# Kernel optimization log

Hardware: AMD Instinct MI355X
Metric: run time of the kernel (lower is better)

Reference implementation:

```python
import jax, jax.numpy as jnp
import numpy as np

B, T, C, H = 4, 2048, 1024, 16
D = C // H          # head_dim = 64
FF = 2 * C          # ff_mult = 2
EPS = 1e-5


def _layernorm(x, g, b):
    mu = jnp.mean(x, axis=-1, keepdims=True)
    var = jnp.mean((x - mu) ** 2, axis=-1, keepdims=True)
    return (x - mu) * jax.lax.rsqrt(var + EPS) * g + b


def setup_inputs() -> dict:
    key = jax.random.key(0)
    ks = jax.random.split(key, 8)
    x = jax.random.normal(ks[0], (B, T, C), dtype=jnp.float32)
    perm = jax.random.permutation(ks[1], T).astype(jnp.int32)
    s_c = 1.0 / np.sqrt(C)
    s_f = 1.0 / np.sqrt(FF)
    Wqkv = jax.random.normal(ks[2], (C, 3 * C), dtype=jnp.float32) * s_c
    Wproj = jax.random.normal(ks[3], (C, C), dtype=jnp.float32) * s_c
    bproj = jnp.zeros((C,), dtype=jnp.float32)
    ln1_g = jnp.ones((C,), dtype=jnp.float32)
    ln1_b = jnp.zeros((C,), dtype=jnp.float32)
    ln2_g = jnp.ones((C,), dtype=jnp.float32)
    ln2_b = jnp.zeros((C,), dtype=jnp.float32)
    Wff1 = jax.random.normal(ks[4], (C, FF), dtype=jnp.float32) * s_c
    bff1 = jnp.zeros((FF,), dtype=jnp.float32)
    Wff2 = jax.random.normal(ks[5], (FF, C), dtype=jnp.float32) * s_f
    bff2 = jnp.zeros((C,), dtype=jnp.float32)
    return {"x": x, "perm": perm, "Wqkv": Wqkv, "Wproj": Wproj, "bproj": bproj,
            "ln1_g": ln1_g, "ln1_b": ln1_b, "ln2_g": ln2_g, "ln2_b": ln2_b,
            "Wff1": Wff1, "bff1": bff1, "Wff2": Wff2, "bff2": bff2}


def reference(x, perm, Wqkv, Wproj, bproj, ln1_g, ln1_b, ln2_g, ln2_b,
              Wff1, bff1, Wff2, bff2):
    # --- attention branch ---
    h = _layernorm(x, ln1_g, ln1_b)                       # [B,T,C]
    qkv = (h @ Wqkv).reshape(B, T, 3, H, D)
    q, k, v = qkv[:, :, 0], qkv[:, :, 1], qkv[:, :, 2]    # [B,T,H,D]
    # random-permuted causal additive mask: masked = ~tril[:, perm]
    rows = jnp.arange(T)[:, None]
    masked = perm[None, :] > rows                          # [T,T] bool
    bias = jnp.where(masked, -jnp.inf, 0.0).astype(x.dtype)
    scale = 1.0 / np.sqrt(D)
    scores = jnp.einsum('bqhd,bkhd->bhqk', q, k) * scale + bias
    attn = jax.nn.softmax(scores, axis=-1)                 # [B,H,T,T]
    y = jnp.einsum('bhqk,bkhd->bqhd', attn, v).reshape(B, T, C)
    x = x + y @ Wproj + bproj
    # --- MLP branch ---
    h2 = _layernorm(x, ln2_g, ln2_b)
    ff = jax.nn.gelu(h2 @ Wff1 + bff1, approximate=False) @ Wff2 + bff2
    return x + ff
```

## Files before the change

kernel.cpp:

```cpp
#include <hip/hip_runtime.h>
#include <math.h>

#define Bb 4
#define Tt 2048
#define Cc 1024
#define Hh 16
#define Dd 64
#define FFf 2048
#define Mrows (Bb*Tt)

typedef _Float16 f16;
typedef _Float16 half8 __attribute__((ext_vector_type(8)));
typedef _Float16 half4 __attribute__((ext_vector_type(4)));
typedef _Float16 half2 __attribute__((ext_vector_type(2)));
typedef __fp16 fp16x2 __attribute__((ext_vector_type(2)));
typedef float floatx4 __attribute__((ext_vector_type(4)));

#define MFMA16(a,b,c)    __builtin_amdgcn_mfma_f32_16x16x32_f16(a,b,c,0,0,0)
#define MFMA16K16(a,b,c) __builtin_amdgcn_mfma_f32_16x16x16f16(a,b,c,0,0,0)

__device__ __forceinline__ void g2l16(const void* g, void* l) {
  __builtin_amdgcn_global_load_lds((__attribute__((address_space(1))) void*)(g),
                                   (__attribute__((address_space(3))) void*)(l),
                                   16, 0, 0);
}

__global__ __launch_bounds__(256) void wt_kernel(const float* __restrict__ W,
                                                 f16* __restrict__ WT,
                                                 const int K, const int N) {
  __shared__ float tile[32][33];
  const int n0 = blockIdx.x * 32, k0 = blockIdx.y * 32;
  const int tx = threadIdx.x, ty = threadIdx.y;
  #pragma unroll
  for (int i = 0; i < 4; i++)
    tile[ty + 8*i][tx] = W[(size_t)(k0 + ty + 8*i) * N + n0 + tx];
  __syncthreads();
  #pragma unroll
  for (int i = 0; i < 4; i++)
    WT[(size_t)(n0 + ty + 8*i) * K + k0 + tx] = (f16)tile[tx][ty + 8*i];
}

__global__ __launch_bounds__(256) void vt_kernel(const f16* __restrict__ V,
                                                 f16* __restrict__ Vt) {
  __shared__ f16 tile[32][33];
  const int bh = blockIdx.z;
  const int t0 = blockIdx.x * 32, d0 = blockIdx.y * 32;
  const int tx = threadIdx.x, ty = threadIdx.y;
  #pragma unroll
  for (int i = 0; i < 4; i++)
    tile[ty + 8*i][tx] = V[((size_t)bh * Tt + t0 + ty + 8*i) * Dd + d0 + tx];
  __syncthreads();
  #pragma unroll
  for (int i = 0; i < 4; i++)
    Vt[((size_t)bh * Dd + d0 + ty + 8*i) * Tt + t0 + tx] = tile[tx][ty + 8*i];
}

__global__ __launch_bounds__(256) void ln_kernel(const float* __restrict__ x,
                                                 const float* __restrict__ gam,
                                                 const float* __restrict__ bet,
                                                 f16* __restrict__ out) {
  const int row = blockIdx.x;
  const int tid = threadIdx.x;
  const float4 v = ((const float4*)(x + (size_t)row * Cc))[tid];
  float s  = v.x + v.y + v.z + v.w;
  float ss = v.x*v.x + v.y*v.y + v.z*v.z + v.w*v.w;
  #pragma unroll
  for (int o = 32; o >= 1; o >>= 1) { s += __shfl_xor(s, o); ss += __shfl_xor(ss, o); }
  __shared__ float ps[4], pss[4];
  if ((tid & 63) == 0) { ps[tid >> 6] = s; pss[tid >> 6] = ss; }
  __syncthreads();
  s  = ps[0] + ps[1] + ps[2] + ps[3];
  ss = pss[0] + pss[1] + pss[2] + pss[3];
  const float mu   = s * (1.0f / Cc);
  const float rstd = rsqrtf(ss * (1.0f / Cc) - mu * mu + 1e-5f);
  const float4 g4 = ((const float4*)gam)[tid];
  const float4 b4 = ((const float4*)bet)[tid];
  half4 o;
  o[0] = (f16)((v.x - mu) * rstd * g4.x + b4.x);
  o[1] = (f16)((v.y - mu) * rstd * g4.y + b4.y);
  o[2] = (f16)((v.z - mu) * rstd * g4.z + b4.z);
  o[3] = (f16)((v.w - mu) * rstd * g4.w + b4.w);
  ((half4*)(out + (size_t)row * Cc))[tid] = o;
}

template <int MODE>
__global__ __launch_bounds__(256, 2) void gemm_kernel(
    const f16* __restrict__ A, const f16* __restrict__ Bt, const int Kdim,
    const float* __restrict__ resid, const float* __restrict__ bias,
    float* __restrict__ outF, f16* __restrict__ outH,
    f16* __restrict__ outQ, f16* __restrict__ outK, f16* __restrict__ outV) {
  __shared__ f16 As[128 * 32];
  __shared__ f16 Bs[128 * 32];
  const int tid = threadIdx.x;
  const int lane = tid & 63;
  const int w = tid >> 6;
  const int wr = w >> 1, wc = w & 1;
  const int bm = blockIdx.y, bn = blockIdx.x;

  floatx4 acc[4][4] = {};

  const size_t aBase = (size_t)(bm*128 + w*32 + (lane >> 2)) * Kdim + (lane & 3) * 8;
  const size_t bBase = (size_t)(bn*128 + w*32 + (lane >> 2)) * Kdim + (lane & 3) * 8;

  for (int ks = 0; ks < Kdim; ks += 32) {
    __syncthreads();
    g2l16(A  + aBase + ks,                    &As[(w*2 + 0) * 512]);
    g2l16(A  + aBase + (size_t)16*Kdim + ks,  &As[(w*2 + 1) * 512]);
    g2l16(Bt + bBase + ks,                    &Bs[(w*2 + 0) * 512]);
    g2l16(Bt + bBase + (size_t)16*Kdim + ks,  &Bs[(w*2 + 1) * 512]);
    __syncthreads();
    half8 aF[4], bF[4];
    #pragma unroll
    for (int mi = 0; mi < 4; mi++)
      aF[mi] = *(const half8*)&As[(wr*64 + mi*16 + (lane & 15)) * 32 + (lane >> 4) * 8];
    #pragma unroll
    for (int ni = 0; ni < 4; ni++)
      bF[ni] = *(const half8*)&Bs[(wc*64 + ni*16 + (lane & 15)) * 32 + (lane >> 4) * 8];
    #pragma unroll
    for (int mi = 0; mi < 4; mi++)
      #pragma unroll
      for (int ni = 0; ni < 4; ni++)
        acc[mi][ni] = MFMA16(aF[mi], bF[ni], acc[mi][ni]);
  }

  const int rowBase = bm*128 + wr*64;
  const int colBase = bn*128 + wc*64;
  #pragma unroll
  for (int mi = 0; mi < 4; mi++) {
    #pragma unroll
    for (int ni = 0; ni < 4; ni++) {
      #pragma unroll
      for (int r = 0; r < 4; r++) {
        const int row = rowBase + mi*16 + (lane >> 4) * 4 + r;
        const int col = colBase + ni*16 + (lane & 15);
        const float vv = acc[mi][ni][r];
        if (MODE == 0) {
          const int s = col >> 10;
          const int hh = (col >> 6) & 15;
          const int d = col & 63;
          const int bI = row >> 11;
          const int t = row & 2047;
          const size_t addr = (((size_t)(bI*Hh + hh)) * Tt + t) * Dd + d;
          f16* dst = (s == 0) ? outQ : (s == 1 ? outK : outV);
          dst[addr] = (f16)(s == 0 ? vv * 0.18033688f : vv);
        } else if (MODE == 1) {
          const size_t a = (size_t)row * Cc + col;
          outF[a] = vv + resid[a] + bias[col];
        } else if (MODE == 2) {
          const float t = vv + bias[col];
          const float gl = 0.5f * t * (1.0f + erff(t * 0.70710678118654752f));
          outH[(size_t)row * FFf + col] = (f16)gl;
        } else {
          const size_t a = (size_t)row * Cc + col;
          outF[a] = vv + bias[col] + resid[a];
        }
      }
    }
  }
}

__global__ __launch_bounds__(256, 4) void attn_kernel(
    const f16* __restrict__ Q, const f16* __restrict__ Kg,
    const f16* __restrict__ Vtg, const int* __restrict__ perm,
    f16* __restrict__ Y) {
  __shared__ f16 Ks[64 * 64];
  __shared__ f16 Vs[64 * 64];
  __shared__ int permS[64];

  const int tid = threadIdx.x;
  const int lane = tid & 63;
  const int w = tid >> 6;
  const int low = lane & 15;
  const int quad = lane >> 4;
  const int bh = blockIdx.y;
  const int q0 = blockIdx.x * 128;
  const int b = bh >> 4, h = bh & 15;

  half8 qF[2][2];
  {
    const size_t base = ((size_t)bh * Tt + q0 + w*32) * Dd;
    #pragma unroll
    for (int qi = 0; qi < 2; qi++)
      #pragma unroll
      for (int kc = 0; kc < 2; kc++)
        qF[qi][kc] = *(const half8*)(Q + base + (size_t)(qi*16 + low) * Dd +
                                     kc*32 + quad*8);
  }

  floatx4 O[4][2] = {};
  float l_[2] = {0.f, 0.f};

  const int gd = ((lane & 7) ^ (lane >> 3)) * 8;
  const int krow = lane >> 3;

  for (int kt = 0; kt < Tt / 64; kt++) {
    const int kbase = kt * 64;
    __syncthreads();
    {
      const size_t kgBase = ((size_t)bh * Tt + kbase) * Dd;
      const size_t vgBase = ((size_t)bh * Dd) * Tt + kbase;
      g2l16(Kg  + kgBase + (size_t)(w*16 + 0 + krow) * Dd + gd, &Ks[(w*2 + 0) * 512]);
      g2l16(Kg  + kgBase + (size_t)(w*16 + 8 + krow) * Dd + gd, &Ks[(w*2 + 1) * 512]);
      g2l16(Vtg + vgBase + (size_t)(w*16 + 0 + krow) * Tt + gd, &Vs[(w*2 + 0) * 512]);
      g2l16(Vtg + vgBase + (size_t)(w*16 + 8 + krow) * Tt + gd, &Vs[(w*2 + 1) * 512]);
      if (tid < 64) permS[tid] = perm[kbase + tid];
    }
    __syncthreads();

    floatx4 S[2][4] = {};
    #pragma unroll
    for (int kc = 0; kc < 2; kc++) {
      #pragma unroll
      for (int ki = 0; ki < 4; ki++) {
        const int key = ki*16 + low;
        const half8 kf = *(const half8*)&Ks[key * 64 + (((kc*4 + quad) ^ (lane & 7)) * 8)];
        S[0][ki] = MFMA16(kf, qF[0][kc], S[0][ki]);
        S[1][ki] = MFMA16(kf, qF[1][kc], S[1][ki]);
      }
    }

    int4 pk[4];
    #pragma unroll
    for (int ki = 0; ki < 4; ki++) pk[ki] = *(const int4*)&permS[ki*16 + quad*4];

    half4 pF[2][4];
    #pragma unroll
    for (int qi = 0; qi < 2; qi++) {
      const int qrow = q0 + w*32 + qi*16 + low;
      #pragma unroll
      for (int ki = 0; ki < 4; ki++) {
        const floatx4 sv = S[qi][ki];
        const float p0 = (pk[ki].x > qrow) ? 0.f : __builtin_amdgcn_exp2f(sv[0]);
        const float p1 = (pk[ki].y > qrow) ? 0.f : __builtin_amdgcn_exp2f(sv[1]);
        const float p2 = (pk[ki].z > qrow) ? 0.f : __builtin_amdgcn_exp2f(sv[2]);
        const float p3 = (pk[ki].w > qrow) ? 0.f : __builtin_amdgcn_exp2f(sv[3]);
        l_[qi] += (p0 + p1) + (p2 + p3);
        const half2 lo = __builtin_bit_cast(half2, __builtin_amdgcn_cvt_pkrtz(p0, p1));
        const half2 hi = __builtin_bit_cast(half2, __builtin_amdgcn_cvt_pkrtz(p2, p3));
        pF[qi][ki] = __builtin_shufflevector(lo, hi, 0, 1, 2, 3);
      }
    }

    #pragma unroll
    for (int ki = 0; ki < 4; ki++) {
      #pragma unroll
      for (int ni = 0; ni < 4; ni++) {
        const half4 vf = *(const half4*)&Vs[(ni*16 + low) * 64 +
                                            (((ki*2 + (quad >> 1)) ^ (lane & 7)) * 8) +
                                            (quad & 1) * 4];
        O[ni][0] = MFMA16K16(vf, pF[0][ki], O[ni][0]);
        O[ni][1] = MFMA16K16(vf, pF[1][ki], O[ni][1]);
      }
    }
  }

  #pragma unroll
  for (int qi = 0; qi < 2; qi++) {
    l_[qi] += __shfl_xor(l_[qi], 16);
    l_[qi] += __shfl_xor(l_[qi], 32);
  }

  #pragma unroll
  for (int qi = 0; qi < 2; qi++) {
    const float linv = 1.0f / l_[qi];
    const int trow = q0 + w*32 + qi*16 + low;
    #pragma unroll
    for (int ni = 0; ni < 4; ni++) {
      half4 o;
      #pragma unroll
      for (int r = 0; r < 4; r++) o[r] = (f16)(O[ni][qi][r] * linv);
      *(half4*)&Y[((size_t)(b * Tt + trow)) * Cc + h*64 + ni*16 + quad*4] = o;
    }
  }
}

extern "C" void kernel_launch(void* const* d_in, const int* in_sizes, int n_in,
                              void* d_out, int out_size, void* d_ws, size_t ws_size,
                              hipStream_t stream) {
  const float* x     = (const float*)d_in[0];
  const int*   perm  = (const int*)d_in[1];
  const float* Wqkv  = (const float*)d_in[2];
  const float* Wproj = (const float*)d_in[3];
  const float* bproj = (const float*)d_in[4];
  const float* ln1g  = (const float*)d_in[5];
  const float* ln1b  = (const float*)d_in[6];
  const float* ln2g  = (const float*)d_in[7];
  const float* ln2b  = (const float*)d_in[8];
  const float* Wff1  = (const float*)d_in[9];
  const float* bff1  = (const float*)d_in[10];
  const float* Wff2  = (const float*)d_in[11];
  const float* bff2  = (const float*)d_in[12];
  float* out = (float*)d_out;

  char* ws = (char*)d_ws;
  size_t off = 0;
  auto alloc = [&](size_t bytes) -> void* {
    void* p = ws + off;
    off += (bytes + 255) & ~(size_t)255;
    return p;
  };
  f16*   h1     = (f16*)alloc((size_t)Mrows * Cc * 2);
  f16*   qb     = (f16*)alloc((size_t)Mrows * Cc * 2);
  f16*   kb     = (f16*)alloc((size_t)Mrows * Cc * 2);
  f16*   vb     = (f16*)alloc((size_t)Mrows * Cc * 2);
  f16*   vt     = (f16*)alloc((size_t)Mrows * Cc * 2);
  f16*   yb     = (f16*)alloc((size_t)Mrows * Cc * 2);
  float* xa     = (float*)alloc((size_t)Mrows * Cc * 4);
  f16*   h2     = (f16*)alloc((size_t)Mrows * Cc * 2);
  f16*   gb     = (f16*)alloc((size_t)Mrows * FFf * 2);
  f16*   WqkvT  = (f16*)alloc((size_t)3 * Cc * Cc * 2);
  f16*   WprojT = (f16*)alloc((size_t)Cc * Cc * 2);
  f16*   Wff1T  = (f16*)alloc((size_t)FFf * Cc * 2);
  f16*   Wff2T  = (f16*)alloc((size_t)Cc * FFf * 2);

  const dim3 blkT(32, 8);
  wt_kernel<<<dim3(3*Cc/32, Cc/32), blkT, 0, stream>>>(Wqkv,  WqkvT,  Cc,  3*Cc);
  wt_kernel<<<dim3(Cc/32,   Cc/32), blkT, 0, stream>>>(Wproj, WprojT, Cc,  Cc);
  wt_kernel<<<dim3(FFf/32,  Cc/32), blkT, 0, stream>>>(Wff1,  Wff1T,  Cc,  FFf);
  wt_kernel<<<dim3(Cc/32,  FFf/32), blkT, 0, stream>>>(Wff2,  Wff2T,  FFf, Cc);

  ln_kernel<<<Mrows, 256, 0, stream>>>(x, ln1g, ln1b, h1);

  gemm_kernel<0><<<dim3(3*Cc/128, Mrows/128), 256, 0, stream>>>(
      h1, WqkvT, Cc, nullptr, nullptr, nullptr, nullptr, qb, kb, vb);

  vt_kernel<<<dim3(Tt/32, Dd/32, Bb*Hh), blkT, 0, stream>>>(vb, vt);

  attn_kernel<<<dim3(Tt/128, Bb*Hh), 256, 0, stream>>>(qb, kb, vt, perm, yb);

  gemm_kernel<1><<<dim3(Cc/128, Mrows/128), 256, 0, stream>>>(
      yb, WprojT, Cc, x, bproj, xa, nullptr, nullptr, nullptr, nullptr);

  ln_kernel<<<Mrows, 256, 0, stream>>>(xa, ln2g, ln2b, h2);

  gemm_kernel<2><<<dim3(FFf/128, Mrows/128), 256, 0, stream>>>(
      h2, Wff1T, Cc, nullptr, bff1, nullptr, gb, nullptr, nullptr, nullptr);

  gemm_kernel<3><<<dim3(Cc/128, Mrows/128), 256, 0, stream>>>(
      gb, Wff2T, FFf, xa, bff2, out, nullptr, nullptr, nullptr, nullptr);
}
```

Before: 460.6 us.

## Fuse V transpose into QKV GEMM epilogue and shrink attention query tile

The QKV GEMM epilogue now writes V directly in a transposed, key-permuted layout, so the separate V transpose kernel and its intermediate buffer go away. The attention kernel processes 64 queries per block instead of 128 and raises its occupancy hint. V fragments are now loaded as one half8 split across two K=16 MFMAs, matching the new in-tile key order. This removes a full read and write pass over V, but each K/V tile is now loaded twice as often from global memory, because each block covers fewer queries.

```diff
diff --git a/kernel.cpp b/kernel.cpp
--- a/kernel.cpp
+++ b/kernel.cpp
@@ -13,7 +13,6 @@
 typedef _Float16 half8 __attribute__((ext_vector_type(8)));
 typedef _Float16 half4 __attribute__((ext_vector_type(4)));
 typedef _Float16 half2 __attribute__((ext_vector_type(2)));
-typedef __fp16 fp16x2 __attribute__((ext_vector_type(2)));
 typedef float floatx4 __attribute__((ext_vector_type(4)));
 
 #define MFMA16(a,b,c)    __builtin_amdgcn_mfma_f32_16x16x32_f16(a,b,c,0,0,0)
@@ -38,21 +37,6 @@
   #pragma unroll
   for (int i = 0; i < 4; i++)
     WT[(size_t)(n0 + ty + 8*i) * K + k0 + tx] = (f16)tile[tx][ty + 8*i];
-}
-
-__global__ __launch_bounds__(256) void vt_kernel(const f16* __restrict__ V,
-                                                 f16* __restrict__ Vt) {
-  __shared__ f16 tile[32][33];
-  const int bh = blockIdx.z;
-  const int t0 = blockIdx.x * 32, d0 = blockIdx.y * 32;
-  const int tx = threadIdx.x, ty = threadIdx.y;
-  #pragma unroll
-  for (int i = 0; i < 4; i++)
-    tile[ty + 8*i][tx] = V[((size_t)bh * Tt + t0 + ty + 8*i) * Dd + d0 + tx];
-  __syncthreads();
-  #pragma unroll
-  for (int i = 0; i < 4; i++)
-    Vt[((size_t)bh * Dd + d0 + ty + 8*i) * Tt + t0 + tx] = tile[tx][ty + 8*i];
 }
 
 __global__ __launch_bounds__(256) void ln_kernel(const float* __restrict__ x,
@@ -125,43 +109,58 @@
 
   const int rowBase = bm*128 + wr*64;
   const int colBase = bn*128 + wc*64;
+  const int quadL = (lane >> 4);
   #pragma unroll
   for (int mi = 0; mi < 4; mi++) {
     #pragma unroll
     for (int ni = 0; ni < 4; ni++) {
-      #pragma unroll
-      for (int r = 0; r < 4; r++) {
-        const int row = rowBase + mi*16 + (lane >> 4) * 4 + r;
-        const int col = colBase + ni*16 + (lane & 15);
-        const float vv = acc[mi][ni][r];
-        if (MODE == 0) {
-          const int s = col >> 10;
-          const int hh = (col >> 6) & 15;
-          const int d = col & 63;
-          const int bI = row >> 11;
-          const int t = row & 2047;
-          const size_t addr = (((size_t)(bI*Hh + hh)) * Tt + t) * Dd + d;
-          f16* dst = (s == 0) ? outQ : (s == 1 ? outK : outV);
-          dst[addr] = (f16)(s == 0 ? vv * 0.18033688f : vv);
-        } else if (MODE == 1) {
-          const size_t a = (size_t)row * Cc + col;
-          outF[a] = vv + resid[a] + bias[col];
-        } else if (MODE == 2) {
-          const float t = vv + bias[col];
-          const float gl = 0.5f * t * (1.0f + erff(t * 0.70710678118654752f));
-          outH[(size_t)row * FFf + col] = (f16)gl;
+      const int col = colBase + ni*16 + (lane & 15);
+      if (MODE == 0) {
+        const int s = col >> 10;
+        const int hh = (col >> 6) & 15;
+        const int d = col & 63;
+        const int row0 = rowBase + mi*16 + quadL*4;
+        const int bI = row0 >> 11;
+        const int t0 = row0 & 2047;
+        if (s == 2) {
+          const size_t addr = (((size_t)(bI*Hh + hh)) * Dd + d) * Tt +
+                              (t0 & ~63) + quadL*16 + ((t0 >> 4) & 3) * 4;
+          half4 o;
+          #pragma unroll
+          for (int r = 0; r < 4; r++) o[r] = (f16)acc[mi][ni][r];
+          *(half4*)&outV[addr] = o;
         } else {
-          const size_t a = (size_t)row * Cc + col;
-          outF[a] = vv + bias[col] + resid[a];
+          f16* dst = (s == 0) ? outQ : outK;
+          const float sc = (s == 0) ? 0.18033688f : 1.0f;
+          #pragma unroll
+          for (int r = 0; r < 4; r++)
+            dst[(((size_t)(bI*Hh + hh)) * Tt + t0 + r) * Dd + d] = (f16)(acc[mi][ni][r] * sc);
+        }
+      } else {
+        #pragma unroll
+        for (int r = 0; r < 4; r++) {
+          const int row = rowBase + mi*16 + quadL*4 + r;
+          const float vv = acc[mi][ni][r];
+          if (MODE == 1) {
+            const size_t a = (size_t)row * Cc + col;
+            outF[a] = vv + resid[a] + bias[col];
+          } else if (MODE == 2) {
+            const float t = vv + bias[col];
+            const float gl = 0.5f * t * (1.0f + erff(t * 0.70710678118654752f));
+            outH[(size_t)row * FFf + col] = (f16)gl;
+          } else {
+            const size_t a = (size_t)row * Cc + col;
+            outF[a] = vv + bias[col] + resid[a];
+          }
         }
       }
     }
   }
 }
 
-__global__ __launch_bounds__(256, 4) void attn_kernel(
+__global__ __launch_bounds__(256, 6) void attn_kernel(
     const f16* __restrict__ Q, const f16* __restrict__ Kg,
-    const f16* __restrict__ Vtg, const int* __restrict__ perm,
+    const f16* __restrict__ Vtp, const int* __restrict__ perm,
     f16* __restrict__ Y) {
   __shared__ f16 Ks[64 * 64];
   __shared__ f16 Vs[64 * 64];
@@ -173,22 +172,19 @@
   const int low = lane & 15;
   const int quad = lane >> 4;
   const int bh = blockIdx.y;
-  const int q0 = blockIdx.x * 128;
+  const int q0 = blockIdx.x * 64;
   const int b = bh >> 4, h = bh & 15;
 
-  half8 qF[2][2];
+  half8 qF[2];
   {
-    const size_t base = ((size_t)bh * Tt + q0 + w*32) * Dd;
-    #pragma unroll
-    for (int qi = 0; qi < 2; qi++)
-      #pragma unroll
-      for (int kc = 0; kc < 2; kc++)
-        qF[qi][kc] = *(const half8*)(Q + base + (size_t)(qi*16 + low) * Dd +
-                                     kc*32 + quad*8);
-  }
-
-  floatx4 O[4][2] = {};
-  float l_[2] = {0.f, 0.f};
+    const size_t base = ((size_t)bh * Tt + q0 + w*16 + low) * Dd;
+    #pragma unroll
+    for (int kc = 0; kc < 2; kc++)
+      qF[kc] = *(const half8*)(Q + base + kc*32 + quad*8);
+  }
+
+  floatx4 O[4] = {};
+  float l_ = 0.f;
 
   const int gd = ((lane & 7) ^ (lane >> 3)) * 8;
   const int krow = lane >> 3;
@@ -201,21 +197,20 @@
       const size_t vgBase = ((size_t)bh * Dd) * Tt + kbase;
       g2l16(Kg  + kgBase + (size_t)(w*16 + 0 + krow) * Dd + gd, &Ks[(w*2 + 0) * 512]);
       g2l16(Kg  + kgBase + (size_t)(w*16 + 8 + krow) * Dd + gd, &Ks[(w*2 + 1) * 512]);
-      g2l16(Vtg + vgBase + (size_t)(w*16 + 0 + krow) * Tt + gd, &Vs[(w*2 + 0) * 512]);
-      g2l16(Vtg + vgBase + (size_t)(w*16 + 8 + krow) * Tt + gd, &Vs[(w*2 + 1) * 512]);
+      g2l16(Vtp + vgBase + (size_t)(w*16 + 0 + krow) * Tt + gd, &Vs[(w*2 + 0) * 512]);
+      g2l16(Vtp + vgBase + (size_t)(w*16 + 8 + krow) * Tt + gd, &Vs[(w*2 + 1) * 512]);
       if (tid < 64) permS[tid] = perm[kbase + tid];
     }
     __syncthreads();
 
-    floatx4 S[2][4] = {};
+    floatx4 S[4] = {};
     #pragma unroll
     for (int kc = 0; kc < 2; kc++) {
       #pragma unroll
       for (int ki = 0; ki < 4; ki++) {
         const int key = ki*16 + low;
         const half8 kf = *(const half8*)&Ks[key * 64 + (((kc*4 + quad) ^ (lane & 7)) * 8)];
-        S[0][ki] = MFMA16(kf, qF[0][kc], S[0][ki]);
-        S[1][ki] = MFMA16(kf, qF[1][kc], S[1][ki]);
+        S[ki] = MFMA16(kf, qF[kc], S[ki]);
       }
     }
 
@@ -223,54 +218,46 @@
     #pragma unroll
     for (int ki = 0; ki < 4; ki++) pk[ki] = *(const int4*)&permS[ki*16 + quad*4];
 
-    half4 pF[2][4];
-    #pragma unroll
-    for (int qi = 0; qi < 2; qi++) {
-      const int qrow = q0 + w*32 + qi*16 + low;
-      #pragma unroll
-      for (int ki = 0; ki < 4; ki++) {
-        const floatx4 sv = S[qi][ki];
-        const float p0 = (pk[ki].x > qrow) ? 0.f : __builtin_amdgcn_exp2f(sv[0]);
-        const float p1 = (pk[ki].y > qrow) ? 0.f : __builtin_amdgcn_exp2f(sv[1]);
-        const float p2 = (pk[ki].z > qrow) ? 0.f : __builtin_amdgcn_exp2f(sv[2]);
-        const float p3 = (pk[ki].w > qrow) ? 0.f : __builtin_amdgcn_exp2f(sv[3]);
-        l_[qi] += (p0 + p1) + (p2 + p3);
-        const half2 lo = __builtin_bit_cast(half2, __builtin_amdgcn_cvt_pkrtz(p0, p1));
-        const half2 hi = __builtin_bit_cast(half2, __builtin_amdgcn_cvt_pkrtz(p2, p3));
-        pF[qi][ki] = __builtin_shufflevector(lo, hi, 0, 1, 2, 3);
-      }
-    }
-
+    const int qrow = q0 + w*16 + low;
+    half4 pF[4];
     #pragma unroll
     for (int ki = 0; ki < 4; ki++) {
+      const floatx4 sv = S[ki];
+      const float p0 = (pk[ki].x > qrow) ? 0.f : __builtin_amdgcn_exp2f(sv[0]);
+      const float p1 = (pk[ki].y > qrow) ? 0.f : __builtin_amdgcn_exp2f(sv[1]);
+      const float p2 = (pk[ki].z > qrow) ? 0.f : __builtin_amdgcn_exp2f(sv[2]);
+      const float p3 = (pk[ki].w > qrow) ? 0.f : __builtin_amdgcn_exp2f(sv[3]);
+      l_ += (p0 + p1) + (p2 + p3);
+      const half2 lo = __builtin_bit_cast(half2, __builtin_amdgcn_cvt_pkrtz(p0, p1));
+      const half2 hi = __builtin_bit_cast(half2, __builtin_amdgcn_cvt_pkrtz(p2, p3));
+      pF[ki] = __builtin_shufflevector(lo, hi, 0, 1, 2, 3);
+    }
+
+    #pragma unroll
+    for (int ki2 = 0; ki2 < 2; ki2++) {
       #pragma unroll
       for (int ni = 0; ni < 4; ni++) {
-        const half4 vf = *(const half4*)&Vs[(ni*16 + low) * 64 +
-                                            (((ki*2 + (quad >> 1)) ^ (lane & 7)) * 8) +
-                                            (quad & 1) * 4];
-        O[ni][0] = MFMA16K16(vf, pF[0][ki], O[ni][0]);
-        O[ni][1] = MFMA16K16(vf, pF[1][ki], O[ni][1]);
+        const int d = ni*16 + low;
+        const half8 v8 = *(const half8*)&Vs[d * 64 + (((quad*2 + ki2) ^ (lane & 7)) * 8)];
+        const half4 vfA = __builtin_shufflevector(v8, v8, 0, 1, 2, 3);
+        const half4 vfB = __builtin_shufflevector(v8, v8, 4, 5, 6, 7);
+        O[ni] = MFMA16K16(vfA, pF[2*ki2 + 0], O[ni]);
+        O[ni] = MFMA16K16(vfB, pF[2*ki2 + 1], O[ni]);
       }
     }
   }
 
-  #pragma unroll
-  for (int qi = 0; qi < 2; qi++) {
-    l_[qi] += __shfl_xor(l_[qi], 16);
-    l_[qi] += __shfl_xor(l_[qi], 32);
-  }
-
-  #pragma unroll
-  for (int qi = 0; qi < 2; qi++) {
-    const float linv = 1.0f / l_[qi];
-    const int trow = q0 + w*32 + qi*16 + low;
-    #pragma unroll
-    for (int ni = 0; ni < 4; ni++) {
-      half4 o;
-      #pragma unroll
-      for (int r = 0; r < 4; r++) o[r] = (f16)(O[ni][qi][r] * linv);
-      *(half4*)&Y[((size_t)(b * Tt + trow)) * Cc + h*64 + ni*16 + quad*4] = o;
-    }
+  l_ += __shfl_xor(l_, 16);
+  l_ += __shfl_xor(l_, 32);
+
+  const float linv = 1.0f / l_;
+  const int trow = q0 + w*16 + low;
+  #pragma unroll
+  for (int ni = 0; ni < 4; ni++) {
+    half4 o;
+    #pragma unroll
+    for (int r = 0; r < 4; r++) o[r] = (f16)(O[ni][r] * linv);
+    *(half4*)&Y[((size_t)(b * Tt + trow)) * Cc + h*64 + ni*16 + quad*4] = o;
   }
 }
 
@@ -302,8 +289,7 @@
   f16*   h1     = (f16*)alloc((size_t)Mrows * Cc * 2);
   f16*   qb     = (f16*)alloc((size_t)Mrows * Cc * 2);
   f16*   kb     = (f16*)alloc((size_t)Mrows * Cc * 2);
-  f16*   vb     = (f16*)alloc((size_t)Mrows * Cc * 2);
-  f16*   vt     = (f16*)alloc((size_t)Mrows * Cc * 2);
+  f16*   vtp    = (f16*)alloc((size_t)Mrows * Cc * 2);
   f16*   yb     = (f16*)alloc((size_t)Mrows * Cc * 2);
   float* xa     = (float*)alloc((size_t)Mrows * Cc * 4);
   f16*   h2     = (f16*)alloc((size_t)Mrows * Cc * 2);
@@ -322,11 +308,9 @@
   ln_kernel<<<Mrows, 256, 0, stream>>>(x, ln1g, ln1b, h1);
 
   gemm_kernel<0><<<dim3(3*Cc/128, Mrows/128), 256, 0, stream>>>(
-      h1, WqkvT, Cc, nullptr, nullptr, nullptr, nullptr, qb, kb, vb);
-
-  vt_kernel<<<dim3(Tt/32, Dd/32, Bb*Hh), blkT, 0, stream>>>(vb, vt);
-
-  attn_kernel<<<dim3(Tt/128, Bb*Hh), 256, 0, stream>>>(qb, kb, vt, perm, yb);
+      h1, WqkvT, Cc, nullptr, nullptr, nullptr, nullptr, qb, kb, vtp);
+
+  attn_kernel<<<dim3(Tt/64, Bb*Hh), 256, 0, stream>>>(qb, kb, vtp, perm, yb);
 
   gemm_kernel<1><<<dim3(Cc/128, Mrows/128), 256, 0, stream>>>(
       yb, WprojT, Cc, x, bproj, xa, nullptr, nullptr, nullptr, nullptr);
```

Result: no change. 465.8 us (+1.1%).
